# Kernel tuning notes

Hardware: AMD Instinct MI355X
Metric: run time of the kernel (lower is better)

Reference implementation:

```python
import jax, jax.numpy as jnp
import numpy as np

EPS = 1e-3  # keras LayerNormalization default epsilon

def setup_inputs() -> dict:
    key = jax.random.key(0)
    k1, k2 = jax.random.split(key)
    B, N, D, M = 16, 4096, 768, 8
    x = jax.random.normal(k1, (B, N, D), dtype=jnp.float32)
    queries = jax.random.normal(k2, (M, D), dtype=jnp.float32)
    gamma = jnp.ones((D,), dtype=jnp.float32)
    beta = jnp.zeros((D,), dtype=jnp.float32)
    return {"x": x, "queries": queries, "gamma": gamma, "beta": beta}

def reference(x, queries, gamma, beta):
    D = x.shape[-1]
    scale = D ** -0.5
    # LayerNorm over last dim (keras default: epsilon=1e-3, learned gamma/beta)
    mu = jnp.mean(x, axis=-1, keepdims=True)
    var = jnp.mean(jnp.square(x - mu), axis=-1, keepdims=True)
    xn = (x - mu) * jax.lax.rsqrt(var + EPS) * gamma + beta  # [B, N, D]
    # sim = queries @ (x^T * scale) -> [B, M, N]
    sim = jnp.einsum('md,bnd->bmn', queries, xn) * scale
    attn = jax.nn.softmax(sim, axis=-1)
    # out = attn @ x_normed -> [B, M, D]
    return jnp.einsum('bmn,bnd->bmd', attn, xn)
```

## Files before the change

kernel.cpp:

```cpp
#include <hip/hip_runtime.h>
#include <hip/hip_bf16.h>


#define B_ 16
#define N_ 4096
#define D_ 768
#define M_ 8
#define EPS_ 1e-3f
#define SCALE_ 0.03608439182435161f

#define SIM_OFF   0
#define MEAN_OFF  524288
#define RSTD_OFF  589824

__global__ __launch_bounds__(256) void k_ln_sim(
    const float* __restrict__ x,
    const float* __restrict__ q,
    const float* __restrict__ gm,
    const float* __restrict__ bt,
    float* __restrict__ sim, float* __restrict__ meanb, float* __restrict__ rstdb)
{
    const int lane = threadIdx.x & 63;
    const int gw   = blockIdx.x * 4 + (threadIdx.x >> 6);
    const int total_waves = gridDim.x * 4;

    float g[12], bb[12], qr[8][12];
#pragma unroll
    for (int i = 0; i < 3; i++) {
        const int c4 = (lane + i * 64) * 4;
        float4 gv = *(const float4*)(gm + c4);
        float4 bv = *(const float4*)(bt + c4);
        g[i * 4 + 0] = gv.x; g[i * 4 + 1] = gv.y; g[i * 4 + 2] = gv.z; g[i * 4 + 3] = gv.w;
        bb[i * 4 + 0] = bv.x; bb[i * 4 + 1] = bv.y; bb[i * 4 + 2] = bv.z; bb[i * 4 + 3] = bv.w;
#pragma unroll
        for (int m = 0; m < 8; m++) {
            float4 qv = *(const float4*)(q + m * D_ + c4);
            qr[m][i * 4 + 0] = qv.x; qr[m][i * 4 + 1] = qv.y;
            qr[m][i * 4 + 2] = qv.z; qr[m][i * 4 + 3] = qv.w;
        }
    }

    for (int row = gw; row < B_ * N_; row += total_waves) {
        const float* xr = x + (size_t)row * D_;
        float v[12];
#pragma unroll
        for (int i = 0; i < 3; i++) {
            float4 p = *(const float4*)(xr + (lane + i * 64) * 4);
            v[i * 4 + 0] = p.x; v[i * 4 + 1] = p.y;
            v[i * 4 + 2] = p.z; v[i * 4 + 3] = p.w;
        }
        float s = 0.f, s2 = 0.f;
#pragma unroll
        for (int k = 0; k < 12; k++) { s += v[k]; s2 += v[k] * v[k]; }
#pragma unroll
        for (int mask = 32; mask; mask >>= 1) {
            s  += __shfl_xor(s,  mask, 64);
            s2 += __shfl_xor(s2, mask, 64);
        }
        const float mean = s * (1.0f / 768.0f);
        float var = s2 * (1.0f / 768.0f) - mean * mean;
        var = fmaxf(var, 0.0f);
        const float rstd = rsqrtf(var + EPS_);

        float acc[8];
#pragma unroll
        for (int m = 0; m < 8; m++) acc[m] = 0.f;
#pragma unroll
        for (int k = 0; k < 12; k++) {
            const float xn = (v[k] - mean) * rstd * g[k] + bb[k];
#pragma unroll
            for (int m = 0; m < 8; m++) acc[m] = fmaf(qr[m][k], xn, acc[m]);
        }
#pragma unroll
        for (int mask = 32; mask; mask >>= 1)
#pragma unroll
            for (int m = 0; m < 8; m++) acc[m] += __shfl_xor(acc[m], mask, 64);

        if (lane == 0) {
            const int b = row >> 12, n = row & (N_ - 1);
            meanb[row] = mean;
            rstdb[row] = rstd;
#pragma unroll
            for (int m = 0; m < 8; m++)
                sim[(size_t)((b * 8 + m) << 12) + n] = acc[m] * SCALE_;
        }
    }
}

__global__ __launch_bounds__(256) void k_softmax(float* __restrict__ sim)
{
    float* p = sim + (size_t)blockIdx.x * N_;
    const int t = threadIdx.x;
    const int lane = t & 63, wave = t >> 6;
    __shared__ float red[4];

    float v[16];
    float mx = -3.4e38f;
#pragma unroll
    for (int i = 0; i < 16; i++) { v[i] = p[t + i * 256]; mx = fmaxf(mx, v[i]); }
#pragma unroll
    for (int mask = 32; mask; mask >>= 1) mx = fmaxf(mx, __shfl_xor(mx, mask, 64));
    if (lane == 0) red[wave] = mx;
    __syncthreads();
    mx = fmaxf(fmaxf(red[0], red[1]), fmaxf(red[2], red[3]));
    __syncthreads();

    float s = 0.f;
#pragma unroll
    for (int i = 0; i < 16; i++) { v[i] = __expf(v[i] - mx); s += v[i]; }
#pragma unroll
    for (int mask = 32; mask; mask >>= 1) s += __shfl_xor(s, mask, 64);
    if (lane == 0) red[wave] = s;
    __syncthreads();
    s = red[0] + red[1] + red[2] + red[3];

    const float inv = 1.0f / s;
#pragma unroll
    for (int i = 0; i < 16; i++) p[t + i * 256] = v[i] * inv;
}

__global__ __launch_bounds__(256) void k_out(
    const float* __restrict__ x,
    const float* __restrict__ gm,
    const float* __restrict__ bt,
    const float* __restrict__ sim,
    const float* __restrict__ meanb,
    const float* __restrict__ rstdb,
    float* __restrict__ out)
{
    __shared__ float attn_s[8 * 256];
    __shared__ float mean_s[256];
    __shared__ float rstd_s[256];

    const int b = blockIdx.x >> 4;
    const int n0 = (blockIdx.x & 15) * 256;
    const int t = threadIdx.x;

#pragma unroll
    for (int k = 0; k < 8; k++) {
        const int idx = t + k * 256;
        attn_s[idx] = sim[(size_t)((b * 8 + (idx >> 8)) << 12) + n0 + (idx & 255)];
    }
    mean_s[t] = meanb[b * N_ + n0 + t];
    rstd_s[t] = rstdb[b * N_ + n0 + t];
    __syncthreads();

    const float g0 = gm[t],       bb0 = bt[t];
    const float g1 = gm[t + 256], bb1 = bt[t + 256];
    const float g2 = gm[t + 512], bb2 = bt[t + 512];

    float acc[8][3];
#pragma unroll
    for (int m = 0; m < 8; m++)
#pragma unroll
        for (int j = 0; j < 3; j++) acc[m][j] = 0.f;

    const float* xb = x + ((size_t)(b * N_ + n0)) * D_;
    for (int nn = 0; nn < 256; nn++) {
        const float* xr = xb + (size_t)nn * D_;
        const float mu = mean_s[nn], rs = rstd_s[nn];
        const float xn0 = (xr[t]       - mu) * rs * g0 + bb0;
        const float xn1 = (xr[t + 256] - mu) * rs * g1 + bb1;
        const float xn2 = (xr[t + 512] - mu) * rs * g2 + bb2;
#pragma unroll
        for (int m = 0; m < 8; m++) {
            const float a = attn_s[m * 256 + nn];
            acc[m][0] = fmaf(a, xn0, acc[m][0]);
            acc[m][1] = fmaf(a, xn1, acc[m][1]);
            acc[m][2] = fmaf(a, xn2, acc[m][2]);
        }
    }

#pragma unroll
    for (int m = 0; m < 8; m++) {
        float* o = out + (size_t)(b * 8 + m) * D_;
        atomicAdd(o + t,       acc[m][0]);
        atomicAdd(o + t + 256, acc[m][1]);
        atomicAdd(o + t + 512, acc[m][2]);
    }
}

extern "C" void kernel_launch(void* const* d_in, const int* in_sizes, int n_in,
                              void* d_out, int out_size, void* d_ws, size_t ws_size,
                              hipStream_t stream)
{
    const float* x  = (const float*)d_in[0];
    const float* q  = (const float*)d_in[1];
    const float* gm = (const float*)d_in[2];
    const float* bt = (const float*)d_in[3];
    float* out = (float*)d_out;

    float* ws    = (float*)d_ws;
    float* sim   = ws + SIM_OFF;
    float* meanb = ws + MEAN_OFF;
    float* rstdb = ws + RSTD_OFF;

    hipMemsetAsync(out, 0, (size_t)B_ * M_ * D_ * sizeof(float), stream);

    k_ln_sim<<<2048, 256, 0, stream>>>(x, q, gm, bt, sim, meanb, rstdb);
    k_softmax<<<B_ * M_, 256, 0, stream>>>(sim);
    k_out<<<B_ * 16, 256, 0, stream>>>(x, gm, bt, sim, meanb, rstdb, out);
}
```

Before: 349.5 us.

## Split softmax into stats pass and fuse normalization into output kernel with more blocks

The softmax kernel now only computes the per-row max and inverse sum. The exponentiation and normalization move into the output kernel's shared-memory staging, which removes a full write-back of the sim matrix. The output kernel's chunk size drops from 256 to 64 rows, so the grid grows from 256 to 1024 blocks. This fills the GPU's compute units better during the bandwidth-bound second pass over x. The cost is four times as many atomicAdds on the output, which is mitigated by staggering the order in which blocks update rows of m.

```diff
diff --git a/kernel.cpp b/kernel.cpp
--- a/kernel.cpp
+++ b/kernel.cpp
@@ -12,6 +12,8 @@
 #define SIM_OFF   0
 #define MEAN_OFF  524288
 #define RSTD_OFF  589824
+#define SMAX_OFF  655360
+#define SINV_OFF  655488
 
 __global__ __launch_bounds__(256) void k_ln_sim(
     const float* __restrict__ x,
@@ -87,9 +89,10 @@
     }
 }
 
-__global__ __launch_bounds__(256) void k_softmax(float* __restrict__ sim)
-{
-    float* p = sim + (size_t)blockIdx.x * N_;
+__global__ __launch_bounds__(256) void k_stats(
+    const float* __restrict__ sim, float* __restrict__ smax, float* __restrict__ sinv)
+{
+    const float* p = sim + (size_t)blockIdx.x * N_;
     const int t = threadIdx.x;
     const int lane = t & 63, wave = t >> 6;
     __shared__ float red[4];
@@ -107,16 +110,16 @@
 
     float s = 0.f;
 #pragma unroll
-    for (int i = 0; i < 16; i++) { v[i] = __expf(v[i] - mx); s += v[i]; }
+    for (int i = 0; i < 16; i++) s += __expf(v[i] - mx);
 #pragma unroll
     for (int mask = 32; mask; mask >>= 1) s += __shfl_xor(s, mask, 64);
     if (lane == 0) red[wave] = s;
     __syncthreads();
-    s = red[0] + red[1] + red[2] + red[3];
-
-    const float inv = 1.0f / s;
-#pragma unroll
-    for (int i = 0; i < 16; i++) p[t + i * 256] = v[i] * inv;
+    if (t == 0) {
+        s = red[0] + red[1] + red[2] + red[3];
+        smax[blockIdx.x] = mx;
+        sinv[blockIdx.x] = 1.0f / s;
+    }
 }
 
 __global__ __launch_bounds__(256) void k_out(
@@ -126,23 +129,29 @@
     const float* __restrict__ sim,
     const float* __restrict__ meanb,
     const float* __restrict__ rstdb,
+    const float* __restrict__ smax,
+    const float* __restrict__ sinv,
     float* __restrict__ out)
 {
-    __shared__ float attn_s[8 * 256];
-    __shared__ float mean_s[256];
-    __shared__ float rstd_s[256];
-
-    const int b = blockIdx.x >> 4;
-    const int n0 = (blockIdx.x & 15) * 256;
+    __shared__ float w_s[8 * 64];
+    __shared__ float mean_s[64];
+    __shared__ float rstd_s[64];
+
+    const int b = blockIdx.x >> 6;
+    const int n0 = (blockIdx.x & 63) * 64;
     const int t = threadIdx.x;
 
 #pragma unroll
-    for (int k = 0; k < 8; k++) {
+    for (int k = 0; k < 2; k++) {
         const int idx = t + k * 256;
-        attn_s[idx] = sim[(size_t)((b * 8 + (idx >> 8)) << 12) + n0 + (idx & 255)];
-    }
-    mean_s[t] = meanb[b * N_ + n0 + t];
-    rstd_s[t] = rstdb[b * N_ + n0 + t];
+        const int m = idx >> 6, nn = idx & 63;
+        const float v = sim[(size_t)((b * 8 + m) << 12) + n0 + nn];
+        w_s[idx] = __expf(v - smax[b * 8 + m]) * sinv[b * 8 + m];
+    }
+    if (t < 64) {
+        mean_s[t] = meanb[b * N_ + n0 + t];
+        rstd_s[t] = rstdb[b * N_ + n0 + t];
+    }
     __syncthreads();
 
     const float g0 = gm[t],       bb0 = bt[t];
@@ -156,7 +165,8 @@
         for (int j = 0; j < 3; j++) acc[m][j] = 0.f;
 
     const float* xb = x + ((size_t)(b * N_ + n0)) * D_;
-    for (int nn = 0; nn < 256; nn++) {
+#pragma unroll 4
+    for (int nn = 0; nn < 64; nn++) {
         const float* xr = xb + (size_t)nn * D_;
         const float mu = mean_s[nn], rs = rstd_s[nn];
         const float xn0 = (xr[t]       - mu) * rs * g0 + bb0;
@@ -164,7 +174,7 @@
         const float xn2 = (xr[t + 512] - mu) * rs * g2 + bb2;
 #pragma unroll
         for (int m = 0; m < 8; m++) {
-            const float a = attn_s[m * 256 + nn];
+            const float a = w_s[m * 64 + nn];
             acc[m][0] = fmaf(a, xn0, acc[m][0]);
             acc[m][1] = fmaf(a, xn1, acc[m][1]);
             acc[m][2] = fmaf(a, xn2, acc[m][2]);
@@ -172,7 +182,8 @@
     }
 
 #pragma unroll
-    for (int m = 0; m < 8; m++) {
+    for (int mm = 0; mm < 8; mm++) {
+        const int m = (mm + (blockIdx.x & 7)) & 7;
         float* o = out + (size_t)(b * 8 + m) * D_;
         atomicAdd(o + t,       acc[m][0]);
         atomicAdd(o + t + 256, acc[m][1]);
@@ -194,10 +205,12 @@
     float* sim   = ws + SIM_OFF;
     float* meanb = ws + MEAN_OFF;
     float* rstdb = ws + RSTD_OFF;
+    float* smax  = ws + SMAX_OFF;
+    float* sinv  = ws + SINV_OFF;
 
     hipMemsetAsync(out, 0, (size_t)B_ * M_ * D_ * sizeof(float), stream);
 
     k_ln_sim<<<2048, 256, 0, stream>>>(x, q, gm, bt, sim, meanb, rstdb);
-    k_softmax<<<B_ * M_, 256, 0, stream>>>(sim);
-    k_out<<<B_ * 16, 256, 0, stream>>>(x, gm, bt, sim, meanb, rstdb, out);
-}
+    k_stats<<<B_ * M_, 256, 0, stream>>>(sim, smax, sinv);
+    k_out<<<B_ * 64, 256, 0, stream>>>(x, gm, bt, sim, meanb, rstdb, smax, sinv, out);
+}
```

Measured after the change: 333.1 us. -4.7%, faster.
